# Performance work log

Measured on AMD Instinct MI355X. Metric: run time of the kernel, lower is better.

## Reference

```python
import math
import jax, jax.numpy as jnp
import numpy as np

B, L, C, E, H, NL, WIN, VOCAB, NC = 2, 1024, 4, 256, 8, 2, 256, 25, 10
HID = 2 * E                      # FFN expansion=2
IN_PAIR = C * (WIN + 1)          # PairwiseContextProjector MLP in_dim


def _sinusoidal_pe(max_len, dim):
    pos = np.arange(max_len, dtype=np.float32)[:, None]
    div = np.exp(np.arange(0, dim, 2, dtype=np.float32) * (-math.log(10000.0) / dim))
    pe = np.zeros((max_len, dim), np.float32)
    pe[:, 0::2] = np.sin(pos * div)
    pe[:, 1::2] = np.cos(pos * div)
    return jnp.asarray(pe)


def setup_inputs() -> dict:
    key = jax.random.key(0)
    ks = iter(jax.random.split(key, 64))
    def rn(shape, scale):
        return jax.random.normal(next(ks), shape, jnp.float32) * scale
    inp = {}
    inp['tokens'] = jax.random.randint(next(ks), (B, L), 0, VOCAB, dtype=jnp.int32)
    inp['x_pairwise'] = rn((B, C, L, L), 1.0)
    inp['bias'] = rn((B, H, L, L), 1.0)
    inp['mask'] = jnp.ones((B, L), jnp.float32)
    inp['token_emb'] = rn((VOCAB, E), 0.02).at[0].set(0.0)  # padding_idx=0
    inp['pe'] = _sinusoidal_pe(L, E)
    inp['pair_w1'] = rn((IN_PAIR, E), IN_PAIR ** -0.5)
    inp['pair_b1'] = jnp.zeros((E,), jnp.float32)
    inp['pair_w2'] = rn((E, E), E ** -0.5)
    inp['pair_b2'] = jnp.zeros((E,), jnp.float32)
    inp['ln1_g'] = jnp.ones((NL, E), jnp.float32)
    inp['ln1_b'] = jnp.zeros((NL, E), jnp.float32)
    for nm in ('wq', 'wk', 'wv', 'wo'):
        inp[nm] = rn((NL, E, E), E ** -0.5)
    for nm in ('bq', 'bk', 'bv', 'bo'):
        inp[nm] = jnp.zeros((NL, E), jnp.float32)
    inp['gate'] = jnp.full((NL, H), 0.5, jnp.float32)   # bias_gate init 0.5
    inp['ln2_g'] = jnp.ones((NL, E), jnp.float32)
    inp['ln2_b'] = jnp.zeros((NL, E), jnp.float32)
    inp['fw1'] = rn((NL, E, HID), E ** -0.5)
    inp['fb1'] = jnp.zeros((NL, HID), jnp.float32)
    inp['fw2'] = rn((NL, HID, E), HID ** -0.5)
    inp['fb2'] = jnp.zeros((NL, E), jnp.float32)
    inp['hln_g'] = jnp.ones((E,), jnp.float32)
    inp['hln_b'] = jnp.zeros((E,), jnp.float32)
    inp['hw1'] = rn((E, E), E ** -0.5)
    inp['hb1'] = jnp.zeros((E,), jnp.float32)
    inp['hw2'] = rn((E, NC), E ** -0.5)
    inp['hb2'] = jnp.zeros((NC,), jnp.float32)
    return inp


def _ln(x, g, b):
    m = x.mean(-1, keepdims=True)
    v = ((x - m) ** 2).mean(-1, keepdims=True)
    return (x - m) / jnp.sqrt(v + 1e-5) * g + b


def _gelu(x):
    return jax.nn.gelu(x, approximate=False)  # torch nn.GELU default = exact erf


def _forward(tokens, x_pairwise, bias, mask, token_emb, pe,
             pair_w1, pair_b1, pair_w2, pair_b2,
             ln1_g, ln1_b, wq, bq, wk, bk, wv, bv, wo, bo, gate,
             ln2_g, ln2_b, fw1, fb1, fw2, fb2,
             hln_g, hln_b, hw1, hb1, hw2, hb2):
    Bx, Lx = tokens.shape
    half = WIN // 2
    padded = jnp.pad(x_pairwise, ((0, 0), (0, 0), (0, 0), (half, half)))
    idx = (jnp.arange(Lx)[:, None] + jnp.arange(WIN + 1)[None, :])[None, None]
    win = jnp.take_along_axis(padded, idx, axis=3)          # [B,C,L,W+1]
    flat = win.transpose(0, 2, 1, 3).reshape(Bx, Lx, C * (WIN + 1))
    pair_ctx = jnp.maximum(flat @ pair_w1 + pair_b1, 0.0) @ pair_w2 + pair_b2

    # SequenceEmbedding + pairwise context
    x = token_emb[tokens] + pe[None, :Lx] + pair_ctx         # [B,L,E]

    D = E // H
    scale = D ** -0.5
    key_bias = (1.0 - mask)[:, None, None, :] * (-10000.0)   # [B,1,1,L]
    for i in range(NL):
        # BiasedMultiHeadAttention (pre-norm + residual)
        xn = _ln(x, ln1_g[i], ln1_b[i])
        Q = (xn @ wq[i] + bq[i]).reshape(Bx, Lx, H, D)
        K = (xn @ wk[i] + bk[i]).reshape(Bx, Lx, H, D)
        V = (xn @ wv[i] + bv[i]).reshape(Bx, Lx, H, D)
        logits = jnp.einsum('blhd,bmhd->bhlm', Q, K) * scale
        logits = logits + gate[i][None, :, None, None] * bias + key_bias
        attn = jax.nn.softmax(logits, axis=-1)
        attn = jnp.nan_to_num(attn) * mask[:, None, :, None]
        out = jnp.einsum('bhlm,bmhd->blhd', attn, V).reshape(Bx, Lx, E)
        out = out * mask[..., None]
        x = x + out @ wo[i] + bo[i]
        # FeedForwardNetwork: x + W2(GELU(W1(LN(x))))
        x = x + _gelu(_ln(x, ln2_g[i], ln2_b[i]) @ fw1[i] + fb1[i]) @ fw2[i] + fb2[i]

    # masked mean pool + ClassificationHead
    pooled = (x * mask[..., None]).sum(1) / jnp.maximum(mask.sum(1, keepdims=True), 1.0)
    h = _ln(pooled, hln_g, hln_b)
    return _gelu(h @ hw1 + hb1) @ hw2 + hb2                  # [B, NC]


def reference(tokens, x_pairwise, bias, mask, token_emb, pe,
              pair_w1, pair_b1, pair_w2, pair_b2,
              ln1_g, ln1_b, wq, bq, wk, bk, wv, bv, wo, bo, gate,
              ln2_g, ln2_b, fw1, fb1, fw2, fb2,
              hln_g, hln_b, hw1, hb1, hw2, hb2):
    return _forward(tokens, x_pairwise, bias, mask, token_emb, pe,
                    pair_w1, pair_b1, pair_w2, pair_b2,
                    ln1_g, ln1_b, wq, bq, wk, bk, wv, bv, wo, bo, gate,
                    ln2_g, ln2_b, fw1, fb1, fw2, fb2,
                    hln_g, hln_b, hw1, hb1, hw2, hb2)
```

## Files before the change

### kernel.cpp

```cpp
#include <hip/hip_runtime.h>
#include <math.h>

#define BB     2
#define LL     1024
#define CC     4
#define EE     256
#define HH     8
#define DD     32
#define NLAYER 2
#define W1N    257
#define INPAIR 1028
#define KP1    1056
#define HIDN   512
#define NCN    10
#define SCALEF 0.17677669529663687f

typedef short bf16x8 __attribute__((ext_vector_type(8)));
typedef float f32x4  __attribute__((ext_vector_type(4)));
typedef unsigned short u16x4 __attribute__((ext_vector_type(4)));
typedef unsigned short u16x8 __attribute__((ext_vector_type(8)));

__device__ __forceinline__ float gelu_f(float x) {
    return 0.5f * x * (1.0f + erff(x * 0.7071067811865475f));
}
__device__ __forceinline__ unsigned short f2bf(float f) {
    unsigned u = __float_as_uint(f);
    u += 0x7fffu + ((u >> 16) & 1u);
    return (unsigned short)(u >> 16);
}

struct PrepDesc {
    const float* src[14];
    int K[14];
    int N[14];
    unsigned long long dst[14];
};

__global__ __launch_bounds__(256) void prep_w(PrepDesc pd, unsigned short* __restrict__ wt)
{
    const int mi = blockIdx.y;
    const int k8 = blockIdx.x;
    const int K = pd.K[mi], N = pd.N[mi];
    const int Kp = (K + 31) & ~31;
    if (k8 * 8 >= Kp) return;
    const float* src = pd.src[mi];
    unsigned short* dst = wt + pd.dst[mi];
    for (int n = threadIdx.x; n < N; n += 256) {
        u16x8 o;
        #pragma unroll
        for (int j = 0; j < 8; ++j) {
            int k = k8 * 8 + j;
            float v = (k < K) ? src[(size_t)k * N + n] : 0.f;
            o[j] = f2bf(v);
        }
        *(u16x8*)(dst + ((size_t)k8 * N + n) * 8) = o;
    }
}

__global__ __launch_bounds__(256) void gather_flat(
    const float* __restrict__ xp, unsigned short* __restrict__ flat)
{
    const int row = blockIdx.x;
    const int b = row >> 10, l = row & 1023;
    const float* base = xp + (size_t)b * CC * LL * LL + (size_t)l * LL;
    for (int kp = threadIdx.x; kp < KP1; kp += 256) {
        float v = 0.f;
        if (kp < INPAIR) {
            int c = kp / W1N;
            int w = kp - c * W1N;
            int col = l + w - 128;
            if (col >= 0 && col < LL) v = base[(size_t)c * LL * LL + col];
        }
        flat[(size_t)row * KP1 + kp] = f2bf(v);
    }
}

__global__ __launch_bounds__(256) void ln_bf16(
    const float* __restrict__ x, const float* __restrict__ g,
    const float* __restrict__ bt, unsigned short* __restrict__ out)
{
    const int row = blockIdx.x * 4 + (threadIdx.x >> 6);
    const int lane = threadIdx.x & 63;
    float4 v = *(const float4*)(x + (size_t)row * EE + lane * 4);
    float s = v.x + v.y + v.z + v.w;
    #pragma unroll
    for (int m = 1; m < 64; m <<= 1) s += __shfl_xor(s, m, 64);
    const float mu = s * (1.0f / 256.0f);
    float q2 = 0.f, d;
    d = v.x - mu; q2 += d * d; d = v.y - mu; q2 += d * d;
    d = v.z - mu; q2 += d * d; d = v.w - mu; q2 += d * d;
    #pragma unroll
    for (int m = 1; m < 64; m <<= 1) q2 += __shfl_xor(q2, m, 64);
    const float rstd = rsqrtf(q2 * (1.0f / 256.0f) + 1e-5f);
    float4 gg = *(const float4*)(g + lane * 4);
    float4 bb = *(const float4*)(bt + lane * 4);
    u16x4 o;
    o[0] = f2bf((v.x - mu) * rstd * gg.x + bb.x);
    o[1] = f2bf((v.y - mu) * rstd * gg.y + bb.y);
    o[2] = f2bf((v.z - mu) * rstd * gg.z + bb.z);
    o[3] = f2bf((v.w - mu) * rstd * gg.w + bb.w);
    *(u16x4*)(out + (size_t)row * EE + lane * 4) = o;
}

template<int KP, int EPI>
__global__ __launch_bounds__(256) void gemm_mfma(
    const unsigned short* __restrict__ A,
    const unsigned short* wt0, const float* b0, void* o0,
    const unsigned short* wt1, const float* b1, void* o1,
    const unsigned short* wt2, const float* b2, void* o2,
    int N,
    const int* __restrict__ tokens, const float* __restrict__ temb,
    const float* __restrict__ pe)
{
    const int t = threadIdx.x;
    const int w = t >> 6, lane = t & 63;
    const int m0 = blockIdx.x * 64 + w * 16;
    const int n0 = blockIdx.y * 16;
    const unsigned short* WT; const float* bias; void* out;
    if (blockIdx.z == 0)      { WT = wt0; bias = b0; out = o0; }
    else if (blockIdx.z == 1) { WT = wt1; bias = b1; out = o1; }
    else                      { WT = wt2; bias = b2; out = o2; }

    const int q = lane >> 4, li = lane & 15;
    const unsigned short* ap = A + (size_t)(m0 + li) * KP + q * 8;
    const unsigned short* bp = WT + ((size_t)q * N + n0 + li) * 8;
    f32x4 acc = {0.f, 0.f, 0.f, 0.f};
    for (int ks = 0; ks < KP / 32; ++ks) {
        bf16x8 av = *(const bf16x8*)(ap + ks * 32);
        bf16x8 bv = *(const bf16x8*)(bp + (size_t)ks * 32 * N);
        acc = __builtin_amdgcn_mfma_f32_16x16x32_bf16(av, bv, acc, 0, 0, 0);
    }

    const int colg = n0 + li;
    const float bb = bias[colg];
    const int rbase = m0 + q * 4;
    #pragma unroll
    for (int r = 0; r < 4; ++r) {
        const int row = rbase + r;
        float v = acc[r] + bb;
        if constexpr (EPI == 0) {
            int b = row >> 10, l = row & 1023;
            int h = colg >> 5, d = colg & 31;
            int bh = b * HH + h;
            unsigned short* op = (unsigned short*)out;
            if (blockIdx.z == 0)
                op[((size_t)bh * LL + l) * DD + d] = f2bf(v);
            else if (blockIdx.z == 1)
                op[(size_t)bh * 32768 + (size_t)(d >> 3) * 8192 + (size_t)l * 8 + (d & 7)] = f2bf(v);
            else
                op[(size_t)bh * 32768 + (size_t)(l >> 3) * 256 + (size_t)d * 8 + (l & 7)] = f2bf(v);
        } else if constexpr (EPI == 1) {
            float* op = (float*)out;
            op[(size_t)row * N + colg] += v;
        } else if constexpr (EPI == 2) {
            ((unsigned short*)out)[(size_t)row * N + colg] = f2bf(gelu_f(v));
        } else if constexpr (EPI == 3) {
            ((unsigned short*)out)[(size_t)row * N + colg] = f2bf(fmaxf(v, 0.f));
        } else {
            int tok = tokens[row];
            v += temb[(size_t)tok * EE + colg] + pe[(size_t)(row & 1023) * EE + colg];
            ((float*)out)[(size_t)row * EE + colg] = v;
        }
    }
}

__global__ __launch_bounds__(256, 4) void attn_part_mfma(
    const unsigned short* __restrict__ qb,
    const unsigned short* __restrict__ kswz,
    const unsigned short* __restrict__ vswz,
    const float* __restrict__ bias, const float* __restrict__ mask,
    const float* __restrict__ gate,
    float* __restrict__ Opart, float* __restrict__ statsM,
    float* __restrict__ statsL)
{
    __shared__ unsigned short Pbuf[4][16][72];
    const int t = threadIdx.x;
    const int wq = t >> 6, lane = t & 63;
    const int li = lane & 15, qd = lane >> 4;
    const int h = blockIdx.y, b = blockIdx.z;
    const int bh = b * HH + h;
    const int qt = blockIdx.x & 15, mc = blockIdx.x >> 4;
    const int q0 = qt * 64 + wq * 16;
    const int mbase = mc * 256;
    const float gh = gate[h];

    const bf16x8 qfrag = *(const bf16x8*)(qb + ((size_t)bh * LL + q0 + li) * DD + qd * 8);

    const unsigned short* kbase = kswz + (size_t)bh * 32768 + (size_t)qd * 8192 + (size_t)li * 8;
    const unsigned short* vbase = vswz + (size_t)bh * 32768 + (size_t)qd * 256 + (size_t)li * 8;
    const float* bp0 = bias + ((size_t)bh * LL + q0 + qd * 4) * LL + li;
    const float* mkp = mask + (size_t)b * LL + li;

    float mrun[4], lrun[4];
    f32x4 o0 = {0.f, 0.f, 0.f, 0.f}, o1 = {0.f, 0.f, 0.f, 0.f};
    #pragma unroll
    for (int r = 0; r < 4; ++r) { mrun[r] = -3.0e38f; lrun[r] = 0.f; }

    float bpre[4][4], kbpre[4];
    #pragma unroll
    for (int ms = 0; ms < 4; ++ms) {
        kbpre[ms] = mkp[mbase + ms * 16];
        #pragma unroll
        for (int r = 0; r < 4; ++r) bpre[ms][r] = bp0[(size_t)r * LL + mbase + ms * 16];
    }

    for (int mtt = 0; mtt < 4; ++mtt) {
        const int m0 = mbase + mtt * 64;
        f32x4 S[4];
        #pragma unroll
        for (int ms = 0; ms < 4; ++ms) {
            bf16x8 kf = *(const bf16x8*)(kbase + (size_t)(m0 + ms * 16) * 8);
            f32x4 z = {0.f, 0.f, 0.f, 0.f};
            S[ms] = __builtin_amdgcn_mfma_f32_16x16x32_bf16(qfrag, kf, z, 0, 0, 0);
        }
        float bc[4][4], kbc[4];
        #pragma unroll
        for (int ms = 0; ms < 4; ++ms) {
            kbc[ms] = (1.0f - kbpre[ms]) * (-10000.0f);
            #pragma unroll
            for (int r = 0; r < 4; ++r) bc[ms][r] = bpre[ms][r];
        }
        if (mtt < 3) {
            #pragma unroll
            for (int ms = 0; ms < 4; ++ms) {
                kbpre[ms] = mkp[m0 + 64 + ms * 16];
                #pragma unroll
                for (int r = 0; r < 4; ++r) bpre[ms][r] = bp0[(size_t)r * LL + m0 + 64 + ms * 16];
            }
        }
        float lg[4][4];
        #pragma unroll
        for (int ms = 0; ms < 4; ++ms)
            #pragma unroll
            for (int r = 0; r < 4; ++r)
                lg[ms][r] = fmaf(S[ms][r], SCALEF, fmaf(gh, bc[ms][r], kbc[ms]));

        float rmax[4];
        #pragma unroll
        for (int r = 0; r < 4; ++r)
            rmax[r] = fmaxf(fmaxf(lg[0][r], lg[1][r]), fmaxf(lg[2][r], lg[3][r]));
        #pragma unroll
        for (int bit = 1; bit < 16; bit <<= 1) {
            #pragma unroll
            for (int r = 0; r < 4; ++r) rmax[r] = fmaxf(rmax[r], __shfl_xor(rmax[r], bit, 64));
        }
        float alpha[4], rsum[4];
        #pragma unroll
        for (int r = 0; r < 4; ++r) {
            float nm = fmaxf(mrun[r], rmax[r]);
            alpha[r] = expf(mrun[r] - nm);
            mrun[r] = nm;
        }
        float p[4][4];
        #pragma unroll
        for (int r = 0; r < 4; ++r) rsum[r] = 0.f;
        #pragma unroll
        for (int ms = 0; ms < 4; ++ms)
            #pragma unroll
            for (int r = 0; r < 4; ++r) {
                p[ms][r] = expf(lg[ms][r] - mrun[r]);
                rsum[r] += p[ms][r];
            }
        #pragma unroll
        for (int bit = 1; bit < 16; bit <<= 1) {
            #pragma unroll
            for (int r = 0; r < 4; ++r) rsum[r] += __shfl_xor(rsum[r], bit, 64);
        }
        #pragma unroll
        for (int r = 0; r < 4; ++r) lrun[r] = lrun[r] * alpha[r] + rsum[r];
        #pragma unroll
        for (int r = 0; r < 4; ++r) { o0[r] *= alpha[r]; o1[r] *= alpha[r]; }
        #pragma unroll
        for (int ms = 0; ms < 4; ++ms)
            #pragma unroll
            for (int r = 0; r < 4; ++r)
                Pbuf[wq][qd * 4 + r][ms * 16 + li] = f2bf(p[ms][r]);
        #pragma unroll
        for (int c = 0; c < 2; ++c) {
            bf16x8 pa = *(const bf16x8*)&Pbuf[wq][li][c * 32 + qd * 8];
            bf16x8 vf0 = *(const bf16x8*)(vbase + (size_t)((m0 >> 3) + c * 4) * 256);
            bf16x8 vf1 = *(const bf16x8*)(vbase + (size_t)((m0 >> 3) + c * 4) * 256 + 16 * 8);
            o0 = __builtin_amdgcn_mfma_f32_16x16x32_bf16(pa, vf0, o0, 0, 0, 0);
            o1 = __builtin_amdgcn_mfma_f32_16x16x32_bf16(pa, vf1, o1, 0, 0, 0);
        }
    }
    const size_t rowg0 = (size_t)(mc * 2 + b) * LL;
    #pragma unroll
    for (int r = 0; r < 4; ++r) {
        const int row = q0 + qd * 4 + r;
        const size_t rg = rowg0 + row;
        Opart[rg * EE + h * DD + li]      = o0[r];
        Opart[rg * EE + h * DD + 16 + li] = o1[r];
        if (li == 0) {
            statsM[rg * HH + h] = mrun[r];
            statsL[rg * HH + h] = lrun[r];
        }
    }
}

__global__ __launch_bounds__(256) void attn_merge(
    const float* __restrict__ Opart, const float* __restrict__ statsM,
    const float* __restrict__ statsL, const float* __restrict__ mask,
    unsigned short* __restrict__ aob)
{
    const int row = blockIdx.x;
    const int e = threadIdx.x;
    const int h = e >> 5;
    float m_[4];
    float M = -3.0e38f;
    #pragma unroll
    for (int mc = 0; mc < 4; ++mc) {
        m_[mc] = statsM[((size_t)mc * 2048 + row) * HH + h];
        M = fmaxf(M, m_[mc]);
    }
    float Lsum = 0.f, V = 0.f;
    #pragma unroll
    for (int mc = 0; mc < 4; ++mc) {
        float sc = expf(m_[mc] - M);
        Lsum = fmaf(statsL[((size_t)mc * 2048 + row) * HH + h], sc, Lsum);
        V = fmaf(Opart[((size_t)mc * 2048 + row) * EE + e], sc, V);
    }
    const float mq = mask[row];
    const float r = (Lsum > 0.f ? V / Lsum : 0.f) * mq * mq;
    aob[(size_t)row * EE + e] = f2bf(r);
}

__global__ __launch_bounds__(256) void pool_part(
    const float* __restrict__ x, const float* __restrict__ mask,
    float* __restrict__ part, float* __restrict__ pmask)
{
    const int ch = blockIdx.x, b = blockIdx.y, t = threadIdx.x;
    const int l0 = ch * 64;
    float s = 0.f, ms = 0.f;
    #pragma unroll 4
    for (int i = 0; i < 64; ++i) {
        int l = l0 + i;
        float mm = mask[b * LL + l];
        s = fmaf(x[((size_t)(b * LL + l)) * EE + t], mm, s);
        ms += mm;
    }
    part[(size_t)(b * 16 + ch) * EE + t] = s;
    if (t == 0) pmask[b * 16 + ch] = ms;
}

__global__ __launch_bounds__(256) void head_kernel(
    const float* __restrict__ part, const float* __restrict__ pmask,
    const float* __restrict__ hg, const float* __restrict__ hb,
    const float* __restrict__ w1, const float* __restrict__ b1,
    const float* __restrict__ w2, const float* __restrict__ b2,
    float* __restrict__ outp)
{
    __shared__ float pn[EE];
    __shared__ float red[4];
    __shared__ float wred[4][NCN];
    const int b = blockIdx.x;
    const int t = threadIdx.x;
    const int wv = t >> 6, lane = t & 63;

    float v = 0.f, msum = 0.f;
    #pragma unroll
    for (int c = 0; c < 16; ++c) {
        v += part[(size_t)(b * 16 + c) * EE + t];
        msum += pmask[b * 16 + c];
    }
    v = v / fmaxf(msum, 1.0f);
    float s = v;
    #pragma unroll
    for (int mm = 1; mm < 64; mm <<= 1) s += __shfl_xor(s, mm, 64);
    if (lane == 0) red[wv] = s;
    __syncthreads();
    const float mu = (red[0] + red[1] + red[2] + red[3]) * (1.0f / 256.0f);
    __syncthreads();
    float d = v - mu;
    float q2 = d * d;
    #pragma unroll
    for (int mm = 1; mm < 64; mm <<= 1) q2 += __shfl_xor(q2, mm, 64);
    if (lane == 0) red[wv] = q2;
    __syncthreads();
    const float var = (red[0] + red[1] + red[2] + red[3]) * (1.0f / 256.0f);
    const float rstd = rsqrtf(var + 1e-5f);
    pn[t] = d * rstd * hg[t] + hb[t];
    __syncthreads();
    float acc = b1[t];
    #pragma unroll 8
    for (int k = 0; k < EE; ++k) acc = fmaf(pn[k], w1[k * EE + t], acc);
    const float g = gelu_f(acc);
    float contrib[NCN];
    #pragma unroll
    for (int c = 0; c < NCN; ++c) contrib[c] = g * w2[(size_t)t * NCN + c];
    #pragma unroll
    for (int mm = 1; mm < 64; mm <<= 1) {
        #pragma unroll
        for (int c = 0; c < NCN; ++c) contrib[c] += __shfl_xor(contrib[c], mm, 64);
    }
    if (lane == 0) {
        #pragma unroll
        for (int c = 0; c < NCN; ++c) wred[wv][c] = contrib[c];
    }
    __syncthreads();
    if (t < NCN)
        outp[b * NCN + t] = b2[t] + wred[0][t] + wred[1][t] + wred[2][t] + wred[3][t];
}

extern "C" void kernel_launch(void* const* d_in, const int* in_sizes, int n_in,
                              void* d_out, int out_size, void* d_ws, size_t ws_size,
                              hipStream_t stream) {
    const int*   tokens = (const int*)  d_in[0];
    const float* xp     = (const float*)d_in[1];
    const float* bias   = (const float*)d_in[2];
    const float* mask   = (const float*)d_in[3];
    const float* temb   = (const float*)d_in[4];
    const float* pe     = (const float*)d_in[5];
    const float* pw1    = (const float*)d_in[6];
    const float* pb1    = (const float*)d_in[7];
    const float* pw2    = (const float*)d_in[8];
    const float* pb2    = (const float*)d_in[9];
    const float* ln1g   = (const float*)d_in[10];
    const float* ln1b   = (const float*)d_in[11];
    const float* wq     = (const float*)d_in[12];
    const float* wk     = (const float*)d_in[13];
    const float* wv     = (const float*)d_in[14];
    const float* wo     = (const float*)d_in[15];
    const float* bq     = (const float*)d_in[16];
    const float* bk     = (const float*)d_in[17];
    const float* bv     = (const float*)d_in[18];
    const float* bo     = (const float*)d_in[19];
    const float* gate   = (const float*)d_in[20];
    const float* ln2g   = (const float*)d_in[21];
    const float* ln2b   = (const float*)d_in[22];
    const float* fw1    = (const float*)d_in[23];
    const float* fb1    = (const float*)d_in[24];
    const float* fw2    = (const float*)d_in[25];
    const float* fb2    = (const float*)d_in[26];
    const float* hlng   = (const float*)d_in[27];
    const float* hlnb   = (const float*)d_in[28];
    const float* hw1    = (const float*)d_in[29];
    const float* hb1    = (const float*)d_in[30];
    const float* hw2    = (const float*)d_in[31];
    const float* hb2    = (const float*)d_in[32];

    float* ws = (float*)d_ws;
    const size_t NTOK = (size_t)BB * LL * EE;
    float* x      = ws;
    float* part   = ws + NTOK;
    float* pmaskp = part + 32 * EE;
    float* Opart  = pmaskp + 64;
    float* statsM = Opart + 4 * NTOK;
    float* statsL = statsM + 65536;
    unsigned short* usp = (unsigned short*)(statsL + 65536);
    usp = (unsigned short*)(((size_t)usp + 15) & ~(size_t)15);
    unsigned short* qb16 = usp;
    unsigned short* kswz = qb16 + NTOK;
    unsigned short* vswz = kswz + NTOK;
    unsigned short* xn   = vswz + NTOK;
    unsigned short* aob  = xn + NTOK;
    unsigned short* ffh  = aob + NTOK;
    unsigned short* ph   = ffh + (size_t)BB * LL * HIDN;
    unsigned short* flat = ph + NTOK;
    unsigned short* wt   = flat + (size_t)BB * LL * KP1;

    const size_t OFF_PW1 = 0;
    const size_t OFF_PW2 = 270336;
    const size_t OFF_QKVO = 335872;
    const size_t OFF_FW1 = 860160;
    const size_t OFF_FW2 = 1122304;

    PrepDesc pd;
    pd.src[0] = pw1;  pd.K[0] = INPAIR; pd.N[0] = EE;  pd.dst[0] = OFF_PW1;
    pd.src[1] = pw2;  pd.K[1] = EE;     pd.N[1] = EE;  pd.dst[1] = OFF_PW2;
    for (int l = 0; l < 2; ++l) {
        const float* srcs[4] = {wq + l * EE * EE, wk + l * EE * EE,
                                wv + l * EE * EE, wo + l * EE * EE};
        for (int wch = 0; wch < 4; ++wch) {
            int mi = 2 + l * 4 + wch;
            pd.src[mi] = srcs[wch]; pd.K[mi] = EE; pd.N[mi] = EE;
            pd.dst[mi] = OFF_QKVO + (size_t)(l * 4 + wch) * 65536;
        }
    }
    for (int l = 0; l < 2; ++l) {
        pd.src[10 + l] = fw1 + (size_t)l * EE * HIDN;
        pd.K[10 + l] = EE;  pd.N[10 + l] = HIDN;
        pd.dst[10 + l] = OFF_FW1 + (size_t)l * 131072;
        pd.src[12 + l] = fw2 + (size_t)l * HIDN * EE;
        pd.K[12 + l] = HIDN; pd.N[12 + l] = EE;
        pd.dst[12 + l] = OFF_FW2 + (size_t)l * 131072;
    }
    prep_w<<<dim3(KP1 / 8, 14), dim3(256), 0, stream>>>(pd, wt);

    gather_flat<<<dim3(2048), dim3(256), 0, stream>>>(xp, flat);
    gemm_mfma<KP1, 3><<<dim3(32, 16, 1), dim3(256), 0, stream>>>(
        flat, wt + OFF_PW1, pb1, ph, nullptr, nullptr, nullptr,
        nullptr, nullptr, nullptr, EE, nullptr, nullptr, nullptr);
    gemm_mfma<EE, 4><<<dim3(32, 16, 1), dim3(256), 0, stream>>>(
        ph, wt + OFF_PW2, pb2, x, nullptr, nullptr, nullptr,
        nullptr, nullptr, nullptr, EE, tokens, temb, pe);

    for (int i = 0; i < NLAYER; ++i) {
        ln_bf16<<<dim3(512), dim3(256), 0, stream>>>(x, ln1g + i * EE, ln1b + i * EE, xn);
        gemm_mfma<EE, 0><<<dim3(32, 16, 3), dim3(256), 0, stream>>>(
            xn,
            wt + OFF_QKVO + (size_t)(i * 4 + 0) * 65536, bq + i * EE, qb16,
            wt + OFF_QKVO + (size_t)(i * 4 + 1) * 65536, bk + i * EE, kswz,
            wt + OFF_QKVO + (size_t)(i * 4 + 2) * 65536, bv + i * EE, vswz,
            EE, nullptr, nullptr, nullptr);
        attn_part_mfma<<<dim3(64, HH, BB), dim3(256), 0, stream>>>(
            qb16, kswz, vswz, bias, mask, gate + i * HH, Opart, statsM, statsL);
        attn_merge<<<dim3(2048), dim3(256), 0, stream>>>(Opart, statsM, statsL, mask, aob);
        gemm_mfma<EE, 1><<<dim3(32, 16, 1), dim3(256), 0, stream>>>(
            aob, wt + OFF_QKVO + (size_t)(i * 4 + 3) * 65536, bo + i * EE, x,
            nullptr, nullptr, nullptr, nullptr, nullptr, nullptr,
            EE, nullptr, nullptr, nullptr);
        ln_bf16<<<dim3(512), dim3(256), 0, stream>>>(x, ln2g + i * EE, ln2b + i * EE, xn);
        gemm_mfma<EE, 2><<<dim3(32, 32, 1), dim3(256), 0, stream>>>(
            xn, wt + OFF_FW1 + (size_t)i * 131072, fb1 + i * HIDN, ffh,
            nullptr, nullptr, nullptr, nullptr, nullptr, nullptr,
            HIDN, nullptr, nullptr, nullptr);
        gemm_mfma<HIDN, 1><<<dim3(32, 16, 1), dim3(256), 0, stream>>>(
            ffh, wt + OFF_FW2 + (size_t)i * 131072, fb2 + i * EE, x,
            nullptr, nullptr, nullptr, nullptr, nullptr, nullptr,
            EE, nullptr, nullptr, nullptr);
    }

    pool_part<<<dim3(16, BB), dim3(256), 0, stream>>>(x, mask, part, pmaskp);
    head_kernel<<<dim3(BB), dim3(256), 0, stream>>>(
        part, pmaskp, hlng, hlnb, hw1, hb1, hw2, hb2, (float*)d_out);

    (void)in_sizes; (void)n_in; (void)out_size; (void)ws_size;
}
```

Before: 332.0 us.

## Fuse LayerNorm into QKV/FFN1 GEMM prologue and merge pool with head

Removes the standalone ln_bf16 kernels. The QKV and FFN1 GEMMs now read fp32 x directly, compute row mean and variance in registers with single-pass sums and a cross-lane shuffle, and normalize to bf16 just before the MFMA. Separately, pool_part and head_kernel become one 1024-thread block per batch. This cuts launch count and the xn round trip through memory. In exchange every GEMM block recomputes LN stats for its rows (16 or 32 column blocks per row tile), the single-pass variance is less numerically robust, and the pool now runs on only 2 blocks.

```diff
diff --git a/kernel.cpp b/kernel.cpp
--- a/kernel.cpp
+++ b/kernel.cpp
@@ -75,42 +75,16 @@
     }
 }
 
-__global__ __launch_bounds__(256) void ln_bf16(
-    const float* __restrict__ x, const float* __restrict__ g,
-    const float* __restrict__ bt, unsigned short* __restrict__ out)
-{
-    const int row = blockIdx.x * 4 + (threadIdx.x >> 6);
-    const int lane = threadIdx.x & 63;
-    float4 v = *(const float4*)(x + (size_t)row * EE + lane * 4);
-    float s = v.x + v.y + v.z + v.w;
-    #pragma unroll
-    for (int m = 1; m < 64; m <<= 1) s += __shfl_xor(s, m, 64);
-    const float mu = s * (1.0f / 256.0f);
-    float q2 = 0.f, d;
-    d = v.x - mu; q2 += d * d; d = v.y - mu; q2 += d * d;
-    d = v.z - mu; q2 += d * d; d = v.w - mu; q2 += d * d;
-    #pragma unroll
-    for (int m = 1; m < 64; m <<= 1) q2 += __shfl_xor(q2, m, 64);
-    const float rstd = rsqrtf(q2 * (1.0f / 256.0f) + 1e-5f);
-    float4 gg = *(const float4*)(g + lane * 4);
-    float4 bb = *(const float4*)(bt + lane * 4);
-    u16x4 o;
-    o[0] = f2bf((v.x - mu) * rstd * gg.x + bb.x);
-    o[1] = f2bf((v.y - mu) * rstd * gg.y + bb.y);
-    o[2] = f2bf((v.z - mu) * rstd * gg.z + bb.z);
-    o[3] = f2bf((v.w - mu) * rstd * gg.w + bb.w);
-    *(u16x4*)(out + (size_t)row * EE + lane * 4) = o;
-}
-
-template<int KP, int EPI>
+template<int KP, int EPI, int AST>
 __global__ __launch_bounds__(256) void gemm_mfma(
-    const unsigned short* __restrict__ A,
+    const void* __restrict__ Ain,
     const unsigned short* wt0, const float* b0, void* o0,
     const unsigned short* wt1, const float* b1, void* o1,
     const unsigned short* wt2, const float* b2, void* o2,
     int N,
     const int* __restrict__ tokens, const float* __restrict__ temb,
-    const float* __restrict__ pe)
+    const float* __restrict__ pe,
+    const float* __restrict__ lng, const float* __restrict__ lnb)
 {
     const int t = threadIdx.x;
     const int w = t >> 6, lane = t & 63;
@@ -122,13 +96,58 @@
     else                      { WT = wt2; bias = b2; out = o2; }
 
     const int q = lane >> 4, li = lane & 15;
-    const unsigned short* ap = A + (size_t)(m0 + li) * KP + q * 8;
     const unsigned short* bp = WT + ((size_t)q * N + n0 + li) * 8;
     f32x4 acc = {0.f, 0.f, 0.f, 0.f};
-    for (int ks = 0; ks < KP / 32; ++ks) {
-        bf16x8 av = *(const bf16x8*)(ap + ks * 32);
-        bf16x8 bv = *(const bf16x8*)(bp + (size_t)ks * 32 * N);
-        acc = __builtin_amdgcn_mfma_f32_16x16x32_bf16(av, bv, acc, 0, 0, 0);
+
+    if constexpr (AST == 0) {
+        const unsigned short* ap = (const unsigned short*)Ain + (size_t)(m0 + li) * KP + q * 8;
+        for (int ks = 0; ks < KP / 32; ++ks) {
+            bf16x8 av = *(const bf16x8*)(ap + ks * 32);
+            bf16x8 bv = *(const bf16x8*)(bp + (size_t)ks * 32 * N);
+            acc = __builtin_amdgcn_mfma_f32_16x16x32_bf16(av, bv, acc, 0, 0, 0);
+        }
+    } else {
+        const float* xr = (const float*)Ain + (size_t)(m0 + li) * EE + q * 8;
+        float afr[64];
+        float s1 = 0.f, s2 = 0.f;
+        #pragma unroll
+        for (int ks = 0; ks < 8; ++ks) {
+            float4 u0 = *(const float4*)(xr + ks * 32);
+            float4 u1 = *(const float4*)(xr + ks * 32 + 4);
+            afr[ks * 8 + 0] = u0.x; afr[ks * 8 + 1] = u0.y;
+            afr[ks * 8 + 2] = u0.z; afr[ks * 8 + 3] = u0.w;
+            afr[ks * 8 + 4] = u1.x; afr[ks * 8 + 5] = u1.y;
+            afr[ks * 8 + 6] = u1.z; afr[ks * 8 + 7] = u1.w;
+            s1 += u0.x + u0.y + u0.z + u0.w + u1.x + u1.y + u1.z + u1.w;
+            s2 = fmaf(u0.x, u0.x, s2); s2 = fmaf(u0.y, u0.y, s2);
+            s2 = fmaf(u0.z, u0.z, s2); s2 = fmaf(u0.w, u0.w, s2);
+            s2 = fmaf(u1.x, u1.x, s2); s2 = fmaf(u1.y, u1.y, s2);
+            s2 = fmaf(u1.z, u1.z, s2); s2 = fmaf(u1.w, u1.w, s2);
+        }
+        s1 += __shfl_xor(s1, 16, 64); s1 += __shfl_xor(s1, 32, 64);
+        s2 += __shfl_xor(s2, 16, 64); s2 += __shfl_xor(s2, 32, 64);
+        const float mu = s1 * (1.0f / 256.0f);
+        const float var = s2 * (1.0f / 256.0f) - mu * mu;
+        const float rstd = rsqrtf(fmaxf(var, 0.f) + 1e-5f);
+        #pragma unroll
+        for (int ks = 0; ks < 8; ++ks) {
+            float4 g0v = *(const float4*)(lng + ks * 32 + q * 8);
+            float4 g1v = *(const float4*)(lng + ks * 32 + q * 8 + 4);
+            float4 bb0 = *(const float4*)(lnb + ks * 32 + q * 8);
+            float4 bb1 = *(const float4*)(lnb + ks * 32 + q * 8 + 4);
+            u16x8 uu;
+            uu[0] = f2bf((afr[ks * 8 + 0] - mu) * rstd * g0v.x + bb0.x);
+            uu[1] = f2bf((afr[ks * 8 + 1] - mu) * rstd * g0v.y + bb0.y);
+            uu[2] = f2bf((afr[ks * 8 + 2] - mu) * rstd * g0v.z + bb0.z);
+            uu[3] = f2bf((afr[ks * 8 + 3] - mu) * rstd * g0v.w + bb0.w);
+            uu[4] = f2bf((afr[ks * 8 + 4] - mu) * rstd * g1v.x + bb1.x);
+            uu[5] = f2bf((afr[ks * 8 + 5] - mu) * rstd * g1v.y + bb1.y);
+            uu[6] = f2bf((afr[ks * 8 + 6] - mu) * rstd * g1v.z + bb1.z);
+            uu[7] = f2bf((afr[ks * 8 + 7] - mu) * rstd * g1v.w + bb1.w);
+            bf16x8 av = *(bf16x8*)&uu;
+            bf16x8 bv = *(const bf16x8*)(bp + (size_t)ks * 32 * N);
+            acc = __builtin_amdgcn_mfma_f32_16x16x32_bf16(av, bv, acc, 0, 0, 0);
+        }
     }
 
     const int colg = n0 + li;
@@ -325,77 +344,76 @@
     aob[(size_t)row * EE + e] = f2bf(r);
 }
 
-__global__ __launch_bounds__(256) void pool_part(
+__global__ __launch_bounds__(1024) void pool_head(
     const float* __restrict__ x, const float* __restrict__ mask,
-    float* __restrict__ part, float* __restrict__ pmask)
-{
-    const int ch = blockIdx.x, b = blockIdx.y, t = threadIdx.x;
-    const int l0 = ch * 64;
-    float s = 0.f, ms = 0.f;
-    #pragma unroll 4
-    for (int i = 0; i < 64; ++i) {
-        int l = l0 + i;
-        float mm = mask[b * LL + l];
-        s = fmaf(x[((size_t)(b * LL + l)) * EE + t], mm, s);
-        ms += mm;
-    }
-    part[(size_t)(b * 16 + ch) * EE + t] = s;
-    if (t == 0) pmask[b * 16 + ch] = ms;
-}
-
-__global__ __launch_bounds__(256) void head_kernel(
-    const float* __restrict__ part, const float* __restrict__ pmask,
     const float* __restrict__ hg, const float* __restrict__ hb,
     const float* __restrict__ w1, const float* __restrict__ b1,
     const float* __restrict__ w2, const float* __restrict__ b2,
     float* __restrict__ outp)
 {
-    __shared__ float pn[EE];
+    __shared__ float psum[4][EE];
+    __shared__ float msums[4];
     __shared__ float red[4];
     __shared__ float wred[4][NCN];
+    __shared__ float pn[EE];
     const int b = blockIdx.x;
     const int t = threadIdx.x;
+    const int col = t & 255, c = t >> 8;
+
+    float s = 0.f, ms = 0.f;
+    for (int i = 0; i < 256; ++i) {
+        int l = c * 256 + i;
+        float mm = mask[b * LL + l];
+        s = fmaf(x[((size_t)b * LL + l) * EE + col], mm, s);
+        ms += mm;
+    }
+    psum[c][col] = s;
+    if (col == 0) msums[c] = ms;
+    __syncthreads();
+
+    float v = 0.f;
     const int wv = t >> 6, lane = t & 63;
-
-    float v = 0.f, msum = 0.f;
-    #pragma unroll
-    for (int c = 0; c < 16; ++c) {
-        v += part[(size_t)(b * 16 + c) * EE + t];
-        msum += pmask[b * 16 + c];
-    }
-    v = v / fmaxf(msum, 1.0f);
-    float s = v;
-    #pragma unroll
-    for (int mm = 1; mm < 64; mm <<= 1) s += __shfl_xor(s, mm, 64);
-    if (lane == 0) red[wv] = s;
+    if (t < EE) {
+        float tot = psum[0][t] + psum[1][t] + psum[2][t] + psum[3][t];
+        float msum = msums[0] + msums[1] + msums[2] + msums[3];
+        v = tot / fmaxf(msum, 1.0f);
+        float sv = v;
+        #pragma unroll
+        for (int mm = 1; mm < 64; mm <<= 1) sv += __shfl_xor(sv, mm, 64);
+        if (lane == 0) red[wv] = sv;
+    }
     __syncthreads();
     const float mu = (red[0] + red[1] + red[2] + red[3]) * (1.0f / 256.0f);
     __syncthreads();
-    float d = v - mu;
-    float q2 = d * d;
-    #pragma unroll
-    for (int mm = 1; mm < 64; mm <<= 1) q2 += __shfl_xor(q2, mm, 64);
-    if (lane == 0) red[wv] = q2;
+    if (t < EE) {
+        float d = v - mu;
+        float q2 = d * d;
+        #pragma unroll
+        for (int mm = 1; mm < 64; mm <<= 1) q2 += __shfl_xor(q2, mm, 64);
+        if (lane == 0) red[wv] = q2;
+    }
     __syncthreads();
     const float var = (red[0] + red[1] + red[2] + red[3]) * (1.0f / 256.0f);
     const float rstd = rsqrtf(var + 1e-5f);
-    pn[t] = d * rstd * hg[t] + hb[t];
+    if (t < EE) pn[t] = (v - mu) * rstd * hg[t] + hb[t];
     __syncthreads();
-    float acc = b1[t];
-    #pragma unroll 8
-    for (int k = 0; k < EE; ++k) acc = fmaf(pn[k], w1[k * EE + t], acc);
-    const float g = gelu_f(acc);
-    float contrib[NCN];
-    #pragma unroll
-    for (int c = 0; c < NCN; ++c) contrib[c] = g * w2[(size_t)t * NCN + c];
-    #pragma unroll
-    for (int mm = 1; mm < 64; mm <<= 1) {
-        #pragma unroll
-        for (int c = 0; c < NCN; ++c) contrib[c] += __shfl_xor(contrib[c], mm, 64);
-    }
-    if (lane == 0) {
-        #pragma unroll
-        for (int c = 0; c < NCN; ++c) wred[wv][c] = contrib[c];
+    if (t < EE) {
+        float acc = b1[t];
+        #pragma unroll 8
+        for (int k = 0; k < EE; ++k) acc = fmaf(pn[k], w1[k * EE + t], acc);
+        const float g = gelu_f(acc);
+        float contrib[NCN];
+        #pragma unroll
+        for (int cc = 0; cc < NCN; ++cc) contrib[cc] = g * w2[(size_t)t * NCN + cc];
+        #pragma unroll
+        for (int mm = 1; mm < 64; mm <<= 1) {
+            #pragma unroll
+            for (int cc = 0; cc < NCN; ++cc) contrib[cc] += __shfl_xor(contrib[cc], mm, 64);
+        }
+        if (lane == 0) {
+            #pragma unroll
+            for (int cc = 0; cc < NCN; ++cc) wred[wv][cc] = contrib[cc];
+        }
     }
     __syncthreads();
     if (t < NCN)
@@ -442,9 +460,7 @@
     float* ws = (float*)d_ws;
     const size_t NTOK = (size_t)BB * LL * EE;
     float* x      = ws;
-    float* part   = ws + NTOK;
-    float* pmaskp = part + 32 * EE;
-    float* Opart  = pmaskp + 64;
+    float* Opart  = ws + NTOK;
     float* statsM = Opart + 4 * NTOK;
     float* statsL = statsM + 65536;
     unsigned short* usp = (unsigned short*)(statsL + 65536);
@@ -452,8 +468,7 @@
     unsigned short* qb16 = usp;
     unsigned short* kswz = qb16 + NTOK;
     unsigned short* vswz = kswz + NTOK;
-    unsigned short* xn   = vswz + NTOK;
-    unsigned short* aob  = xn + NTOK;
+    unsigned short* aob  = vswz + NTOK;
     unsigned short* ffh  = aob + NTOK;
     unsigned short* ph   = ffh + (size_t)BB * LL * HIDN;
     unsigned short* flat = ph + NTOK;
@@ -488,42 +503,39 @@
     prep_w<<<dim3(KP1 / 8, 14), dim3(256), 0, stream>>>(pd, wt);
 
     gather_flat<<<dim3(2048), dim3(256), 0, stream>>>(xp, flat);
-    gemm_mfma<KP1, 3><<<dim3(32, 16, 1), dim3(256), 0, stream>>>(
+    gemm_mfma<KP1, 3, 0><<<dim3(32, 16, 1), dim3(256), 0, stream>>>(
         flat, wt + OFF_PW1, pb1, ph, nullptr, nullptr, nullptr,
-        nullptr, nullptr, nullptr, EE, nullptr, nullptr, nullptr);
-    gemm_mfma<EE, 4><<<dim3(32, 16, 1), dim3(256), 0, stream>>>(
+        nullptr, nullptr, nullptr, EE, nullptr, nullptr, nullptr, nullptr, nullptr);
+    gemm_mfma<EE, 4, 0><<<dim3(32, 16, 1), dim3(256), 0, stream>>>(
         ph, wt + OFF_PW2, pb2, x, nullptr, nullptr, nullptr,
-        nullptr, nullptr, nullptr, EE, tokens, temb, pe);
+        nullptr, nullptr, nullptr, EE, tokens, temb, pe, nullptr, nullptr);
 
     for (int i = 0; i < NLAYER; ++i) {
-        ln_bf16<<<dim3(512), dim3(256), 0, stream>>>(x, ln1g + i * EE, ln1b + i * EE, xn);
-        gemm_mfma<EE, 0><<<dim3(32, 16, 3), dim3(256), 0, stream>>>(
-            xn,
+        gemm_mfma<EE, 0, 1><<<dim3(32, 16, 3), dim3(256), 0, stream>>>(
+            x,
             wt + OFF_QKVO + (size_t)(i * 4 + 0) * 65536, bq + i * EE, qb16,
             wt + OFF_QKVO + (size_t)(i * 4 + 1) * 65536, bk + i * EE, kswz,
             wt + OFF_QKVO + (size_t)(i * 4 + 2) * 65536, bv + i * EE, vswz,
-            EE, nullptr, nullptr, nullptr);
+            EE, nullptr, nullptr, nullptr, ln1g + i * EE, ln1b + i * EE);
         attn_part_mfma<<<dim3(64, HH, BB), dim3(256), 0, stream>>>(
             qb16, kswz, vswz, bias, mask, gate + i * HH, Opart, statsM, statsL);
         attn_merge<<<dim3(2048), dim3(256), 0, stream>>>(Opart, statsM, statsL, mask, aob);
-        gemm_mfma<EE, 1><<<dim3(32, 16, 1), dim3(256), 0, stream>>>(
+        gemm_mfma<EE, 1, 0><<<dim3(32, 16, 1), dim3(256), 0, stream>>>(
             aob, wt + OFF_QKVO + (size_t)(i * 4 + 3) * 65536, bo + i * EE, x,
             nullptr, nullptr, nullptr, nullptr, nullptr, nullptr,
-            EE, nullptr, nullptr, nullptr);
-        ln_bf16<<<dim3(512), dim3(256), 0, stream>>>(x, ln2g + i * EE, ln2b + i * EE, xn);
-        gemm_mfma<EE, 2><<<dim3(32, 32, 1), dim3(256), 0, stream>>>(
-            xn, wt + OFF_FW1 + (size_t)i * 131072, fb1 + i * HIDN, ffh,
+            EE, nullptr, nullptr, nullptr, nullptr, nullptr);
+        gemm_mfma<EE, 2, 1><<<dim3(32, 32, 1), dim3(256), 0, stream>>>(
+            x, wt + OFF_FW1 + (size_t)i * 131072, fb1 + i * HIDN, ffh,
             nullptr, nullptr, nullptr, nullptr, nullptr, nullptr,
-            HIDN, nullptr, nullptr, nullptr);
-        gemm_mfma<HIDN, 1><<<dim3(32, 16, 1), dim3(256), 0, stream>>>(
+            HIDN, nullptr, nullptr, nullptr, ln2g + i * EE, ln2b + i * EE);
+        gemm_mfma<HIDN, 1, 0><<<dim3(32, 16, 1), dim3(256), 0, stream>>>(
             ffh, wt + OFF_FW2 + (size_t)i * 131072, fb2 + i * EE, x,
             nullptr, nullptr, nullptr, nullptr, nullptr, nullptr,
-            EE, nullptr, nullptr, nullptr);
-    }
-
-    pool_part<<<dim3(16, BB), dim3(256), 0, stream>>>(x, mask, part, pmaskp);
-    head_kernel<<<dim3(BB), dim3(256), 0, stream>>>(
-        part, pmaskp, hlng, hlnb, hw1, hb1, hw2, hb2, (float*)d_out);
+            EE, nullptr, nullptr, nullptr, nullptr, nullptr);
+    }
+
+    pool_head<<<dim3(BB), dim3(1024), 0, stream>>>(
+        x, mask, hlng, hlnb, hw1, hb1, hw2, hb2, (float*)d_out);
 
     (void)in_sizes; (void)n_in; (void)out_size; (void)ws_size;
 }
```

New measurement: 369.5 us. 1.11x slower.

## Transpose attention scores via LDS so each lane owns one query row

Applied to the files above, without the earlier changes.

The attention kernel now writes the QK^T MFMA output to a float LDS buffer and reads it back transposed, so each lane holds 16 contiguous logits of a single query row. Bias and mask then load as float4 vectors, row max and sum need only two cross-lane shuffles instead of four per row, and the P fragments for the PV MFMA are packed directly in registers without an LDS round trip. The weight-prep and pairwise-gather kernels are merged into one launch, and the workspace reuses ph as the LN output buffer. The trade-offs are an fp32 LDS write/read of S in place of the bf16 P buffer, per-row alpha broadcasts through shuffles, and loss of the prefetch of the next tile's bias.

```diff
diff --git a/kernel.cpp b/kernel.cpp
--- a/kernel.cpp
+++ b/kernel.cpp
@@ -36,42 +36,42 @@
     unsigned long long dst[14];
 };
 
-__global__ __launch_bounds__(256) void prep_w(PrepDesc pd, unsigned short* __restrict__ wt)
-{
-    const int mi = blockIdx.y;
-    const int k8 = blockIdx.x;
-    const int K = pd.K[mi], N = pd.N[mi];
-    const int Kp = (K + 31) & ~31;
-    if (k8 * 8 >= Kp) return;
-    const float* src = pd.src[mi];
-    unsigned short* dst = wt + pd.dst[mi];
-    for (int n = threadIdx.x; n < N; n += 256) {
-        u16x8 o;
-        #pragma unroll
-        for (int j = 0; j < 8; ++j) {
-            int k = k8 * 8 + j;
-            float v = (k < K) ? src[(size_t)k * N + n] : 0.f;
-            o[j] = f2bf(v);
-        }
-        *(u16x8*)(dst + ((size_t)k8 * N + n) * 8) = o;
-    }
-}
-
-__global__ __launch_bounds__(256) void gather_flat(
+__global__ __launch_bounds__(256) void prep_gather(
+    PrepDesc pd, unsigned short* __restrict__ wt,
     const float* __restrict__ xp, unsigned short* __restrict__ flat)
 {
-    const int row = blockIdx.x;
-    const int b = row >> 10, l = row & 1023;
-    const float* base = xp + (size_t)b * CC * LL * LL + (size_t)l * LL;
-    for (int kp = threadIdx.x; kp < KP1; kp += 256) {
-        float v = 0.f;
-        if (kp < INPAIR) {
-            int c = kp / W1N;
-            int w = kp - c * W1N;
-            int col = l + w - 128;
-            if (col >= 0 && col < LL) v = base[(size_t)c * LL * LL + col];
-        }
-        flat[(size_t)row * KP1 + kp] = f2bf(v);
+    const int bid = blockIdx.x;
+    if (bid < 1848) {
+        const int mi = bid / 132, k8 = bid - mi * 132;
+        const int K = pd.K[mi], N = pd.N[mi];
+        const int Kp = (K + 31) & ~31;
+        if (k8 * 8 >= Kp) return;
+        const float* src = pd.src[mi];
+        unsigned short* dst = wt + pd.dst[mi];
+        for (int n = threadIdx.x; n < N; n += 256) {
+            u16x8 o;
+            #pragma unroll
+            for (int j = 0; j < 8; ++j) {
+                int k = k8 * 8 + j;
+                float v = (k < K) ? src[(size_t)k * N + n] : 0.f;
+                o[j] = f2bf(v);
+            }
+            *(u16x8*)(dst + ((size_t)k8 * N + n) * 8) = o;
+        }
+    } else {
+        const int row = bid - 1848;
+        const int b = row >> 10, l = row & 1023;
+        const float* base = xp + (size_t)b * CC * LL * LL + (size_t)l * LL;
+        for (int kp = threadIdx.x; kp < KP1; kp += 256) {
+            float v = 0.f;
+            if (kp < INPAIR) {
+                int c = kp / W1N;
+                int w = kp - c * W1N;
+                int col = l + w - 128;
+                if (col >= 0 && col < LL) v = base[(size_t)c * LL * LL + col];
+            }
+            flat[(size_t)row * KP1 + kp] = f2bf(v);
+        }
     }
 }
 
@@ -173,7 +173,7 @@
     float* __restrict__ Opart, float* __restrict__ statsM,
     float* __restrict__ statsL)
 {
-    __shared__ unsigned short Pbuf[4][16][72];
+    __shared__ float Sbuf[4][16][68];
     const int t = threadIdx.x;
     const int wq = t >> 6, lane = t & 63;
     const int li = lane & 15, qd = lane >> 4;
@@ -185,27 +185,24 @@
     const float gh = gate[h];
 
     const bf16x8 qfrag = *(const bf16x8*)(qb + ((size_t)bh * LL + q0 + li) * DD + qd * 8);
-
     const unsigned short* kbase = kswz + (size_t)bh * 32768 + (size_t)qd * 8192 + (size_t)li * 8;
     const unsigned short* vbase = vswz + (size_t)bh * 32768 + (size_t)qd * 256 + (size_t)li * 8;
-    const float* bp0 = bias + ((size_t)bh * LL + q0 + qd * 4) * LL + li;
-    const float* mkp = mask + (size_t)b * LL + li;
-
-    float mrun[4], lrun[4];
+    const float* brow = bias + ((size_t)bh * LL + q0 + li) * LL;
+    const float* mrow = mask + (size_t)b * LL;
+
+    float mrun = -3.0e38f, lrun = 0.f;
     f32x4 o0 = {0.f, 0.f, 0.f, 0.f}, o1 = {0.f, 0.f, 0.f, 0.f};
-    #pragma unroll
-    for (int r = 0; r < 4; ++r) { mrun[r] = -3.0e38f; lrun[r] = 0.f; }
-
-    float bpre[4][4], kbpre[4];
-    #pragma unroll
-    for (int ms = 0; ms < 4; ++ms) {
-        kbpre[ms] = mkp[mbase + ms * 16];
-        #pragma unroll
-        for (int r = 0; r < 4; ++r) bpre[ms][r] = bp0[(size_t)r * LL + mbase + ms * 16];
-    }
 
     for (int mtt = 0; mtt < 4; ++mtt) {
         const int m0 = mbase + mtt * 64;
+        float4 bv0 = *(const float4*)(brow + m0 + qd * 8);
+        float4 bv1 = *(const float4*)(brow + m0 + qd * 8 + 4);
+        float4 bv2 = *(const float4*)(brow + m0 + 32 + qd * 8);
+        float4 bv3 = *(const float4*)(brow + m0 + 32 + qd * 8 + 4);
+        float4 mk0 = *(const float4*)(mrow + m0 + qd * 8);
+        float4 mk1 = *(const float4*)(mrow + m0 + qd * 8 + 4);
+        float4 mk2 = *(const float4*)(mrow + m0 + 32 + qd * 8);
+        float4 mk3 = *(const float4*)(mrow + m0 + 32 + qd * 8 + 4);
         f32x4 S[4];
         #pragma unroll
         for (int ms = 0; ms < 4; ++ms) {
@@ -213,75 +210,68 @@
             f32x4 z = {0.f, 0.f, 0.f, 0.f};
             S[ms] = __builtin_amdgcn_mfma_f32_16x16x32_bf16(qfrag, kf, z, 0, 0, 0);
         }
-        float bc[4][4], kbc[4];
-        #pragma unroll
-        for (int ms = 0; ms < 4; ++ms) {
-            kbc[ms] = (1.0f - kbpre[ms]) * (-10000.0f);
-            #pragma unroll
-            for (int r = 0; r < 4; ++r) bc[ms][r] = bpre[ms][r];
-        }
-        if (mtt < 3) {
-            #pragma unroll
-            for (int ms = 0; ms < 4; ++ms) {
-                kbpre[ms] = mkp[m0 + 64 + ms * 16];
-                #pragma unroll
-                for (int r = 0; r < 4; ++r) bpre[ms][r] = bp0[(size_t)r * LL + m0 + 64 + ms * 16];
-            }
-        }
-        float lg[4][4];
         #pragma unroll
         for (int ms = 0; ms < 4; ++ms)
             #pragma unroll
             for (int r = 0; r < 4; ++r)
-                lg[ms][r] = fmaf(S[ms][r], SCALEF, fmaf(gh, bc[ms][r], kbc[ms]));
-
-        float rmax[4];
-        #pragma unroll
-        for (int r = 0; r < 4; ++r)
-            rmax[r] = fmaxf(fmaxf(lg[0][r], lg[1][r]), fmaxf(lg[2][r], lg[3][r]));
-        #pragma unroll
-        for (int bit = 1; bit < 16; bit <<= 1) {
-            #pragma unroll
-            for (int r = 0; r < 4; ++r) rmax[r] = fmaxf(rmax[r], __shfl_xor(rmax[r], bit, 64));
-        }
-        float alpha[4], rsum[4];
+                Sbuf[wq][qd * 4 + r][ms * 16 + li] = S[ms][r];
+        float4 s0 = *(const float4*)&Sbuf[wq][li][qd * 8];
+        float4 s1 = *(const float4*)&Sbuf[wq][li][qd * 8 + 4];
+        float4 s2 = *(const float4*)&Sbuf[wq][li][32 + qd * 8];
+        float4 s3 = *(const float4*)&Sbuf[wq][li][32 + qd * 8 + 4];
+        float lg[16];
+        lg[0]  = fmaf(s0.x, SCALEF, fmaf(gh, bv0.x, (1.0f - mk0.x) * -10000.0f));
+        lg[1]  = fmaf(s0.y, SCALEF, fmaf(gh, bv0.y, (1.0f - mk0.y) * -10000.0f));
+        lg[2]  = fmaf(s0.z, SCALEF, fmaf(gh, bv0.z, (1.0f - mk0.z) * -10000.0f));
+        lg[3]  = fmaf(s0.w, SCALEF, fmaf(gh, bv0.w, (1.0f - mk0.w) * -10000.0f));
+        lg[4]  = fmaf(s1.x, SCALEF, fmaf(gh, bv1.x, (1.0f - mk1.x) * -10000.0f));
+        lg[5]  = fmaf(s1.y, SCALEF, fmaf(gh, bv1.y, (1.0f - mk1.y) * -10000.0f));
+        lg[6]  = fmaf(s1.z, SCALEF, fmaf(gh, bv1.z, (1.0f - mk1.z) * -10000.0f));
+        lg[7]  = fmaf(s1.w, SCALEF, fmaf(gh, bv1.w, (1.0f - mk1.w) * -10000.0f));
+        lg[8]  = fmaf(s2.x, SCALEF, fmaf(gh, bv2.x, (1.0f - mk2.x) * -10000.0f));
+        lg[9]  = fmaf(s2.y, SCALEF, fmaf(gh, bv2.y, (1.0f - mk2.y) * -10000.0f));
+        lg[10] = fmaf(s2.z, SCALEF, fmaf(gh, bv2.z, (1.0f - mk2.z) * -10000.0f));
+        lg[11] = fmaf(s2.w, SCALEF, fmaf(gh, bv2.w, (1.0f - mk2.w) * -10000.0f));
+        lg[12] = fmaf(s3.x, SCALEF, fmaf(gh, bv3.x, (1.0f - mk3.x) * -10000.0f));
+        lg[13] = fmaf(s3.y, SCALEF, fmaf(gh, bv3.y, (1.0f - mk3.y) * -10000.0f));
+        lg[14] = fmaf(s3.z, SCALEF, fmaf(gh, bv3.z, (1.0f - mk3.z) * -10000.0f));
+        lg[15] = fmaf(s3.w, SCALEF, fmaf(gh, bv3.w, (1.0f - mk3.w) * -10000.0f));
+        float tm = lg[0];
+        #pragma unroll
+        for (int j = 1; j < 16; ++j) tm = fmaxf(tm, lg[j]);
+        tm = fmaxf(tm, __shfl_xor(tm, 16, 64));
+        tm = fmaxf(tm, __shfl_xor(tm, 32, 64));
+        const float nm = fmaxf(mrun, tm);
+        const float alpha = expf(mrun - nm);
+        mrun = nm;
+        float p[16];
+        float ts = 0.f;
+        #pragma unroll
+        for (int j = 0; j < 16; ++j) { p[j] = expf(lg[j] - nm); ts += p[j]; }
+        ts += __shfl_xor(ts, 16, 64);
+        ts += __shfl_xor(ts, 32, 64);
+        lrun = lrun * alpha + ts;
         #pragma unroll
         for (int r = 0; r < 4; ++r) {
-            float nm = fmaxf(mrun[r], rmax[r]);
-            alpha[r] = expf(mrun[r] - nm);
-            mrun[r] = nm;
-        }
-        float p[4][4];
-        #pragma unroll
-        for (int r = 0; r < 4; ++r) rsum[r] = 0.f;
-        #pragma unroll
-        for (int ms = 0; ms < 4; ++ms)
-            #pragma unroll
-            for (int r = 0; r < 4; ++r) {
-                p[ms][r] = expf(lg[ms][r] - mrun[r]);
-                rsum[r] += p[ms][r];
-            }
-        #pragma unroll
-        for (int bit = 1; bit < 16; bit <<= 1) {
-            #pragma unroll
-            for (int r = 0; r < 4; ++r) rsum[r] += __shfl_xor(rsum[r], bit, 64);
-        }
-        #pragma unroll
-        for (int r = 0; r < 4; ++r) lrun[r] = lrun[r] * alpha[r] + rsum[r];
-        #pragma unroll
-        for (int r = 0; r < 4; ++r) { o0[r] *= alpha[r]; o1[r] *= alpha[r]; }
-        #pragma unroll
-        for (int ms = 0; ms < 4; ++ms)
-            #pragma unroll
-            for (int r = 0; r < 4; ++r)
-                Pbuf[wq][qd * 4 + r][ms * 16 + li] = f2bf(p[ms][r]);
-        #pragma unroll
-        for (int c = 0; c < 2; ++c) {
-            bf16x8 pa = *(const bf16x8*)&Pbuf[wq][li][c * 32 + qd * 8];
-            bf16x8 vf0 = *(const bf16x8*)(vbase + (size_t)((m0 >> 3) + c * 4) * 256);
-            bf16x8 vf1 = *(const bf16x8*)(vbase + (size_t)((m0 >> 3) + c * 4) * 256 + 16 * 8);
-            o0 = __builtin_amdgcn_mfma_f32_16x16x32_bf16(pa, vf0, o0, 0, 0, 0);
-            o1 = __builtin_amdgcn_mfma_f32_16x16x32_bf16(pa, vf1, o1, 0, 0, 0);
+            const float al = __shfl(alpha, qd * 4 + r, 64);
+            o0[r] *= al; o1[r] *= al;
+        }
+        u16x8 pu0, pu1;
+        #pragma unroll
+        for (int j = 0; j < 8; ++j) { pu0[j] = f2bf(p[j]); pu1[j] = f2bf(p[8 + j]); }
+        const bf16x8 pa0 = *(bf16x8*)&pu0;
+        const bf16x8 pa1 = *(bf16x8*)&pu1;
+        {
+            const unsigned short* v0p = vbase + (size_t)((m0 >> 3) + 0) * 256;
+            const unsigned short* v1p = vbase + (size_t)((m0 >> 3) + 4) * 256;
+            bf16x8 vf00 = *(const bf16x8*)(v0p);
+            bf16x8 vf01 = *(const bf16x8*)(v0p + 16 * 8);
+            bf16x8 vf10 = *(const bf16x8*)(v1p);
+            bf16x8 vf11 = *(const bf16x8*)(v1p + 16 * 8);
+            o0 = __builtin_amdgcn_mfma_f32_16x16x32_bf16(pa0, vf00, o0, 0, 0, 0);
+            o1 = __builtin_amdgcn_mfma_f32_16x16x32_bf16(pa0, vf01, o1, 0, 0, 0);
+            o0 = __builtin_amdgcn_mfma_f32_16x16x32_bf16(pa1, vf10, o0, 0, 0, 0);
+            o1 = __builtin_amdgcn_mfma_f32_16x16x32_bf16(pa1, vf11, o1, 0, 0, 0);
         }
     }
     const size_t rowg0 = (size_t)(mc * 2 + b) * LL;
@@ -291,10 +281,11 @@
         const size_t rg = rowg0 + row;
         Opart[rg * EE + h * DD + li]      = o0[r];
         Opart[rg * EE + h * DD + 16 + li] = o1[r];
-        if (li == 0) {
-            statsM[rg * HH + h] = mrun[r];
-            statsL[rg * HH + h] = lrun[r];
-        }
+    }
+    if (qd == 0) {
+        const size_t rg = rowg0 + q0 + li;
+        statsM[rg * HH + h] = mrun;
+        statsL[rg * HH + h] = lrun;
     }
 }
 
@@ -442,18 +433,17 @@
     float* ws = (float*)d_ws;
     const size_t NTOK = (size_t)BB * LL * EE;
     float* x      = ws;
-    float* part   = ws + NTOK;
-    float* pmaskp = part + 32 * EE;
-    float* Opart  = pmaskp + 64;
+    float* Opart  = ws + NTOK;
     float* statsM = Opart + 4 * NTOK;
     float* statsL = statsM + 65536;
-    unsigned short* usp = (unsigned short*)(statsL + 65536);
+    float* part   = statsL + 65536;
+    float* pmaskp = part + 32 * EE;
+    unsigned short* usp = (unsigned short*)(pmaskp + 32);
     usp = (unsigned short*)(((size_t)usp + 15) & ~(size_t)15);
     unsigned short* qb16 = usp;
     unsigned short* kswz = qb16 + NTOK;
     unsigned short* vswz = kswz + NTOK;
-    unsigned short* xn   = vswz + NTOK;
-    unsigned short* aob  = xn + NTOK;
+    unsigned short* aob  = vswz + NTOK;
     unsigned short* ffh  = aob + NTOK;
     unsigned short* ph   = ffh + (size_t)BB * LL * HIDN;
     unsigned short* flat = ph + NTOK;
@@ -485,9 +475,9 @@
         pd.K[12 + l] = HIDN; pd.N[12 + l] = EE;
         pd.dst[12 + l] = OFF_FW2 + (size_t)l * 131072;
     }
-    prep_w<<<dim3(KP1 / 8, 14), dim3(256), 0, stream>>>(pd, wt);
-
-    gather_flat<<<dim3(2048), dim3(256), 0, stream>>>(xp, flat);
+
+    prep_gather<<<dim3(1848 + 2048), dim3(256), 0, stream>>>(pd, wt, xp, flat);
+
     gemm_mfma<KP1, 3><<<dim3(32, 16, 1), dim3(256), 0, stream>>>(
         flat, wt + OFF_PW1, pb1, ph, nullptr, nullptr, nullptr,
         nullptr, nullptr, nullptr, EE, nullptr, nullptr, nullptr);
@@ -496,6 +486,7 @@
         nullptr, nullptr, nullptr, EE, tokens, temb, pe);
 
     for (int i = 0; i < NLAYER; ++i) {
+        unsigned short* xn = ph;
         ln_bf16<<<dim3(512), dim3(256), 0, stream>>>(x, ln1g + i * EE, ln1b + i * EE, xn);
         gemm_mfma<EE, 0><<<dim3(32, 16, 3), dim3(256), 0, stream>>>(
             xn,
```

Result: no change. 330.8 us (-0.4%).
